# Performance work log

Hardware: AMD Instinct MI355X
Metric: run time of the kernel (lower is better)

## Reference

```python
import jax, jax.numpy as jnp
import numpy as np

THETA = 10000.0
D_K = 64
NUM_HEADS = 16


def _rope_tables(token_positions):
    # token_positions: [s] int -> cos/sin: [s, d_k//2]
    pos = token_positions.astype(jnp.float32)
    dim_idx = jnp.arange(0, D_K, 2, dtype=jnp.float32)
    freqs = 1.0 / (THETA ** (dim_idx / D_K))  # [d_k//2]
    ang = pos[:, None] * freqs[None, :]       # [s, d_k//2]
    return jnp.cos(ang), jnp.sin(ang)


def _apply_rope(x, cos, sin):
    # x: [b, h, s, d_k]; cos/sin: [s, d_k//2] broadcast over b, h
    x1 = x[..., 0::2]
    x2 = x[..., 1::2]
    r1 = x1 * cos - x2 * sin
    r2 = x2 * cos + x1 * sin
    return jnp.stack([r1, r2], axis=-1).reshape(x.shape)


def setup_inputs() -> dict:
    key = jax.random.key(0)
    ks = jax.random.split(key, 5)
    b, s, d = 2, 2048, 1024
    x = jax.random.normal(ks[0], (b, s, d), dtype=jnp.float32)
    token_positions = jnp.arange(s, dtype=jnp.int32)
    scale = (2.0 / (d + d)) ** 0.5
    Wq = jax.random.normal(ks[1], (d, d), dtype=jnp.float32) * scale
    Wk = jax.random.normal(ks[2], (d, d), dtype=jnp.float32) * scale
    Wv = jax.random.normal(ks[3], (d, d), dtype=jnp.float32) * scale
    Wo = jax.random.normal(ks[4], (d, d), dtype=jnp.float32) * scale
    return {"x": x, "token_positions": token_positions,
            "Wq": Wq, "Wk": Wk, "Wv": Wv, "Wo": Wo}


def reference(x, token_positions, Wq, Wk, Wv, Wo):
    b, s, d_model = x.shape
    h, d_k = NUM_HEADS, D_K

    def split_heads(t):
        return t.reshape(b, s, h, d_k).transpose(0, 2, 1, 3)  # [b, h, s, d_k]

    Q = split_heads(jnp.einsum('ij,bsj->bsi', Wq, x))
    K = split_heads(jnp.einsum('ij,bsj->bsi', Wk, x))
    V = split_heads(jnp.einsum('ij,bsj->bsi', Wv, x))

    cos, sin = _rope_tables(token_positions)
    Q = _apply_rope(Q, cos, sin)
    K = _apply_rope(K, cos, sin)

    scale = 1.0 / jnp.sqrt(jnp.float32(d_k))
    scores = jnp.einsum('bhqd,bhkd->bhqk', Q, K) * scale  # [b, h, s, s]
    causal = jnp.tril(jnp.ones((s, s), dtype=bool))
    scores = jnp.where(causal, scores, -jnp.inf)
    attn = jax.nn.softmax(scores, axis=-1)
    out = jnp.einsum('bhqk,bhkd->bhqd', attn, V)
    out = out.transpose(0, 2, 1, 3).reshape(b, s, d_model)
    return jnp.einsum('ij,bsj->bsi', Wo, out)
```

## Files before the change

### kernel.cpp

```cpp
#include <hip/hip_runtime.h>
#include <hip/hip_bf16.h>


typedef __attribute__((ext_vector_type(8))) __bf16 bf16x8;
typedef __attribute__((ext_vector_type(4))) float f32x4;
typedef __attribute__((ext_vector_type(16))) float f32x16;
typedef __attribute__((ext_vector_type(4))) int int4v;
typedef __attribute__((ext_vector_type(2))) unsigned int uint2v;

#define MFMA16(a, b, c) __builtin_amdgcn_mfma_f32_16x16x32_bf16(a, b, c, 0, 0, 0)
#define MFMA32(a, b, c) __builtin_amdgcn_mfma_f32_32x32x16_bf16(a, b, c, 0, 0, 0)

__device__ inline unsigned short f2b(float f) {
  unsigned u = __builtin_bit_cast(unsigned, f);
  u = (u + 0x7FFF + ((u >> 16) & 1)) >> 16;
  return (unsigned short)u;
}

__device__ inline unsigned pk2b(float lo, float hi) {
  return (unsigned)f2b(lo) | ((unsigned)f2b(hi) << 16);
}

__device__ inline unsigned cvtpk(float lo, float hi) {
  unsigned r;
  asm("v_cvt_pk_bf16_f32 %0, %1, %2" : "=v"(r) : "v"(lo), "v"(hi));
  return r;
}

__device__ inline void plswap(unsigned a, unsigned b, unsigned& o0, unsigned& o1) {
#if __has_builtin(__builtin_amdgcn_permlane32_swap)
  auto r = __builtin_amdgcn_permlane32_swap(a, b, false, false);
  o0 = r[0];
  o1 = r[1];
#else
  unsigned sa = (unsigned)__shfl_xor((int)a, 32, 64);
  unsigned sb = (unsigned)__shfl_xor((int)b, 32, 64);
  bool hi = (threadIdx.x & 32) != 0;
  o0 = hi ? sb : a;
  o1 = hi ? b : sa;
#endif
}

__device__ inline float fexp2(float x) {
#if __has_builtin(__builtin_amdgcn_exp2f)
  return __builtin_amdgcn_exp2f(x);
#else
  return exp2f(x);
#endif
}


__device__ inline void cvt4(const float* __restrict__ s, unsigned short* __restrict__ d,
                            int i, float sc) {
  float4 v = *(const float4*)(s + i);
  uint2v p = {pk2b(v.x * sc, v.y * sc), pk2b(v.z * sc, v.w * sc)};
  *(uint2v*)(d + i) = p;
}

__global__ __launch_bounds__(256) void prep_kernel(
    const float* __restrict__ x, const float* __restrict__ Wq,
    const float* __restrict__ Wk, const float* __restrict__ Wv,
    const float* __restrict__ Wo, const int* __restrict__ tp,
    unsigned short* __restrict__ xb, unsigned short* __restrict__ Wqkvb,
    unsigned short* __restrict__ Wob, float* __restrict__ cosT,
    float* __restrict__ sinT) {
  int t = blockIdx.x * 256 + threadIdx.x;
  if (t < 1048576) {
    cvt4(x, xb, t * 4, 1.0f);
  } else if (t < 1310720) {
    cvt4(Wq, Wqkvb, (t - 1048576) * 4, 0.18033688f);
  } else if (t < 1572864) {
    cvt4(Wk, Wqkvb + 1048576, (t - 1310720) * 4, 1.0f);
  } else if (t < 1835008) {
    cvt4(Wv, Wqkvb + 2097152, (t - 1572864) * 4, 1.0f);
  } else if (t < 2097152) {
    cvt4(Wo, Wob, (t - 1835008) * 4, 1.0f);
  } else {
    int base = (t - 2097152) * 4;
#pragma unroll
    for (int j = 0; j < 4; ++j) {
      int idx = base + j;
      int p = idx >> 5, i = idx & 31;
      float pos = (float)tp[p];
      float freq = powf(10000.0f, -(float)i / 32.0f);
      float ang = pos * freq;
      cosT[idx] = cosf(ang);
      sinT[idx] = sinf(ang);
    }
  }
}


__device__ __forceinline__ void g_stage(const unsigned short* __restrict__ A,
                                        const unsigned short* __restrict__ B,
                                        unsigned short* __restrict__ As,
                                        unsigned short* __restrict__ Bs,
                                        int m0, int n0, int k0, int w, int lane) {
  const int srow = lane >> 3;
  const int schunk = (lane & 7) ^ srow;
#pragma unroll
  for (int c = 0; c < 4; ++c) {
    const int rb = w * 32 + c * 8;
    const unsigned short* ga = A + (size_t)(m0 + rb + srow) * 1024 + k0 + schunk * 8;
    __builtin_amdgcn_global_load_lds(
        (const __attribute__((address_space(1))) void*)ga,
        (__attribute__((address_space(3))) void*)(As + rb * 64), 16, 0, 0);
    const int rl = rb + srow;
    const int rB = n0 + (rl & 96) + ((rl & 15) << 1) + ((rl >> 4) & 1);
    const unsigned short* gb = B + (size_t)rB * 1024 + k0 + schunk * 8;
    __builtin_amdgcn_global_load_lds(
        (const __attribute__((address_space(1))) void*)gb,
        (__attribute__((address_space(3))) void*)(Bs + rb * 64), 16, 0, 0);
  }
}


__global__ __launch_bounds__(256) void gemm_qkv_kernel(
    const unsigned short* __restrict__ A,
    const unsigned short* __restrict__ B,
    unsigned short* __restrict__ Qb, unsigned short* __restrict__ Kb,
    unsigned short* __restrict__ VbT,
    const float* __restrict__ cosT, const float* __restrict__ sinT) {
  __shared__ unsigned short As[2][128 * 64];
  __shared__ unsigned short Bs[2][128 * 64];
  const int bid = blockIdx.x;
  const int sw = (bid & 7) * 96 + (bid >> 3);
  const int n0 = (sw % 24) * 128, m0 = (sw / 24) * 128;
  const int tid = threadIdx.x, w = tid >> 6, lane = tid & 63;
  const int l15 = lane & 15, l4 = lane >> 4;
  const int wr = w >> 1, wc = w & 1;

  f32x4 acc[4][4] = {};

  g_stage(A, B, As[0], Bs[0], m0, n0, 0, w, lane);
  asm volatile("s_waitcnt vmcnt(0)" ::: "memory");
  __builtin_amdgcn_s_barrier();

  int cur = 0;
  for (int k0 = 0; k0 < 1024; k0 += 64) {
    if (k0 + 64 < 1024)
      g_stage(A, B, As[cur ^ 1], Bs[cur ^ 1], m0, n0, k0 + 64, w, lane);
#pragma unroll
    for (int kk = 0; kk < 2; ++kk) {
      bf16x8 af[4], bfr[4];
#pragma unroll
      for (int m = 0; m < 4; m++) {
        const int row = wr * 64 + m * 16 + l15;
        af[m] = *(const bf16x8*)(&As[cur][row * 64 + (((kk * 4 + l4) ^ (l15 & 7)) * 8)]);
      }
#pragma unroll
      for (int n = 0; n < 4; n++) {
        const int row = wc * 64 + n * 16 + l15;
        bfr[n] = *(const bf16x8*)(&Bs[cur][row * 64 + (((kk * 4 + l4) ^ (l15 & 7)) * 8)]);
      }
#pragma unroll
      for (int m = 0; m < 4; m++)
#pragma unroll
        for (int n = 0; n < 4; n++)
          acc[m][n] = MFMA16(af[m], bfr[n], acc[m][n]);
    }
    asm volatile("s_waitcnt vmcnt(0)" ::: "memory");
    __builtin_amdgcn_s_barrier();
    cur ^= 1;
  }

  const int cbase = n0 & 1023;
  if (n0 < 2048) {
    unsigned short* dst = (n0 < 1024) ? Qb : Kb;
#pragma unroll
    for (int m = 0; m < 4; m++) {
      const int row0 = m0 + wr * 64 + m * 16 + l4 * 4;
#pragma unroll
      for (int k = 0; k < 2; k++) {
        const int col = cbase + wc * 64 + k * 32 + 2 * l15;
        const int pi = k * 16 + l15;
#pragma unroll
        for (int r = 0; r < 4; r++) {
          const int pos = (row0 + r) & 2047;
          float c = cosT[pos * 32 + pi], s = sinT[pos * 32 + pi];
          float v0 = acc[m][2 * k][r], v1 = acc[m][2 * k + 1][r];
          float r1 = fmaf(v0, c, -v1 * s);
          float r2 = fmaf(v1, c, v0 * s);
          *(unsigned*)(dst + (size_t)(row0 + r) * 1024 + col) = pk2b(r1, r2);
        }
      }
    }
  } else {
#pragma unroll
    for (int m = 0; m < 4; m++) {
      const int row0 = m0 + wr * 64 + m * 16 + l4 * 4;
      const int bb = row0 >> 11, seq = row0 & 2047;
#pragma unroll
      for (int k = 0; k < 2; k++) {
        const int dkg = cbase + wc * 64 + k * 32 + 2 * l15;
        const int h = dkg >> 6, dk = dkg & 63;
        unsigned short* vp = VbT + (size_t)(bb * 16 + h) * 131072 + dk * 2048 + seq;
        uint2v e = {pk2b(acc[m][2 * k][0], acc[m][2 * k][1]),
                    pk2b(acc[m][2 * k][2], acc[m][2 * k][3])};
        *(uint2v*)vp = e;
        uint2v o = {pk2b(acc[m][2 * k + 1][0], acc[m][2 * k + 1][1]),
                    pk2b(acc[m][2 * k + 1][2], acc[m][2 * k + 1][3])};
        *(uint2v*)(vp + 2048) = o;
      }
    }
  }
}


__global__ __launch_bounds__(256) void gemm_out_kernel(
    const unsigned short* __restrict__ A,
    const unsigned short* __restrict__ B,
    float* __restrict__ out) {
  __shared__ unsigned short As[2][128 * 64];
  __shared__ unsigned short Bs[2][128 * 64];
  const int bid = blockIdx.x;
  const int sw = (bid & 7) * 32 + (bid >> 3);
  const int n0 = (sw % 8) * 128, m0 = (sw / 8) * 128;
  const int tid = threadIdx.x, w = tid >> 6, lane = tid & 63;
  const int l15 = lane & 15, l4 = lane >> 4;
  const int wr = w >> 1, wc = w & 1;

  f32x4 acc[4][4] = {};

  g_stage(A, B, As[0], Bs[0], m0, n0, 0, w, lane);
  asm volatile("s_waitcnt vmcnt(0)" ::: "memory");
  __builtin_amdgcn_s_barrier();

  int cur = 0;
  for (int k0 = 0; k0 < 1024; k0 += 64) {
    if (k0 + 64 < 1024)
      g_stage(A, B, As[cur ^ 1], Bs[cur ^ 1], m0, n0, k0 + 64, w, lane);
#pragma unroll
    for (int kk = 0; kk < 2; ++kk) {
      bf16x8 af[4], bfr[4];
#pragma unroll
      for (int m = 0; m < 4; m++) {
        const int row = wr * 64 + m * 16 + l15;
        af[m] = *(const bf16x8*)(&As[cur][row * 64 + (((kk * 4 + l4) ^ (l15 & 7)) * 8)]);
      }
#pragma unroll
      for (int n = 0; n < 4; n++) {
        const int row = wc * 64 + n * 16 + l15;
        bfr[n] = *(const bf16x8*)(&Bs[cur][row * 64 + (((kk * 4 + l4) ^ (l15 & 7)) * 8)]);
      }
#pragma unroll
      for (int m = 0; m < 4; m++)
#pragma unroll
        for (int n = 0; n < 4; n++)
          acc[m][n] = MFMA16(af[m], bfr[n], acc[m][n]);
    }
    asm volatile("s_waitcnt vmcnt(0)" ::: "memory");
    __builtin_amdgcn_s_barrier();
    cur ^= 1;
  }

#pragma unroll
  for (int m = 0; m < 4; m++) {
    const int row0 = m0 + wr * 64 + m * 16 + l4 * 4;
#pragma unroll
    for (int k = 0; k < 2; k++) {
      const int col = n0 + wc * 64 + k * 32 + 2 * l15;
#pragma unroll
      for (int r = 0; r < 4; r++) {
        float2 v = {acc[m][2 * k][r], acc[m][2 * k + 1][r]};
        *(float2*)(out + (size_t)(row0 + r) * 1024 + col) = v;
      }
    }
  }
}


__device__ __forceinline__ void stage_tiles(const unsigned short* __restrict__ Kgb,
                                            const unsigned short* __restrict__ Vgb,
                                            unsigned short* KsBuf, unsigned short* VsBuf,
                                            int kv0, int w, int lane) {
#pragma unroll
  for (int c = 0; c < 2; ++c) {
    const int rowbase = w * 16 + c * 8;
    const int row = rowbase + (lane >> 3);
    const int chunk = (lane & 7) ^ (lane >> 3);
    const unsigned short* gk = Kgb + (size_t)(kv0 + row) * 1024 + chunk * 8;
    __builtin_amdgcn_global_load_lds(
        (const __attribute__((address_space(1))) void*)gk,
        (__attribute__((address_space(3))) void*)(KsBuf + rowbase * 64), 16, 0, 0);
    const unsigned short* gv = Vgb + (size_t)row * 2048 + kv0 + chunk * 8;
    __builtin_amdgcn_global_load_lds(
        (const __attribute__((address_space(1))) void*)gv,
        (__attribute__((address_space(3))) void*)(VsBuf + rowbase * 64), 16, 0, 0);
  }
}

__global__ __launch_bounds__(256) void attn_kernel(
    const unsigned short* __restrict__ Qb,
    const unsigned short* __restrict__ Kb,
    const unsigned short* __restrict__ VbT,
    unsigned short* __restrict__ Ob) {
  __shared__ unsigned short Ks[3][64 * 64];
  __shared__ unsigned short Vs[3][64 * 64];
  const int bh = blockIdx.x;
  const int y = blockIdx.y;
  const int qt = (y < 8) ? (15 - 2 * y) : (2 * (y - 8));
  const int b = bh >> 4, h = bh & 15;
  const int tid = threadIdx.x, w = tid >> 6, lane = tid & 63;
  const int l31 = lane & 31, l32 = lane >> 5;
  const int sw = l31 & 7;

  const unsigned short* qptr =
      Qb + (size_t)(b * 2048 + qt * 128 + w * 32 + l31) * 1024 + h * 64 + l32 * 8;
  bf16x8 qa[4];
#pragma unroll
  for (int kk = 0; kk < 4; ++kk) qa[kk] = *(const bf16x8*)(qptr + kk * 16);

  f32x16 oacc[2] = {};
  float m = -3e38f, l = 0.f;

  const unsigned short* Kgb = Kb + (size_t)b * 2048 * 1024 + h * 64;
  const unsigned short* Vgb = VbT + (size_t)bh * 131072;

  const int nt = 2 * qt + 2;
  stage_tiles(Kgb, Vgb, Ks[0], Vs[0], 0, w, lane);
  stage_tiles(Kgb, Vgb, Ks[1], Vs[1], 64, w, lane);

  int ib = 0, is_ = 2;
  for (int t = 0; t < nt; ++t) {
    if (t < nt - 1) {
      asm volatile("s_waitcnt vmcnt(4)" ::: "memory");
    } else {
      asm volatile("s_waitcnt vmcnt(0)" ::: "memory");
    }
    __builtin_amdgcn_s_barrier();
    __builtin_amdgcn_sched_barrier(0);
    if (t + 2 < nt)
      stage_tiles(Kgb, Vgb, Ks[is_], Vs[is_], (t + 2) * 64, w, lane);

    const char* ksb = (const char*)Ks[ib];
    f32x16 st[2];
    __builtin_amdgcn_s_setprio(1);
#pragma unroll
    for (int f = 0; f < 2; ++f) {
      const char* kb = ksb + (f * 32 + l31) * 128;
      f32x16 z = {};
#pragma unroll
      for (int kk = 0; kk < 4; ++kk) {
        bf16x8 kf = *(const bf16x8*)(kb + ((((kk << 1) | l32) ^ sw) * 16));
        z = MFMA32(kf, qa[kk], z);
      }
      st[f] = z;
    }
    __builtin_amdgcn_s_setprio(0);

    if (t >= 2 * qt + (w >> 1)) {
      const int qg = qt * 128 + w * 32 + l31;
      const int kvb = t * 64 + 4 * l32;
#pragma unroll
      for (int f = 0; f < 2; ++f)
#pragma unroll
        for (int reg = 0; reg < 16; ++reg) {
          int kv = kvb + 32 * f + (reg & 3) + 8 * (reg >> 2);
          if (kv > qg) st[f][reg] = -3e38f;
        }
    }

    float a8[8];
#pragma unroll
    for (int j = 0; j < 8; ++j)
      a8[j] = fmaxf(fmaxf(st[0][j], st[0][j + 8]), fmaxf(st[1][j], st[1][j + 8]));
    float pm = fmaxf(fmaxf(fmaxf(a8[0], a8[1]), fmaxf(a8[2], a8[3])),
                     fmaxf(fmaxf(a8[4], a8[5]), fmaxf(a8[6], a8[7])));
    pm = fmaxf(pm, __shfl_xor(pm, 32, 64));

    if (!__all(pm - m <= 8.0f)) {
      float mn = fmaxf(m, pm);
      float al = fexp2(m - mn);
      l *= al;
#pragma unroll
      for (int df = 0; df < 2; ++df)
#pragma unroll
        for (int reg = 0; reg < 16; ++reg) oacc[df][reg] *= al;
      m = mn;
    }

    unsigned pku[2][4][2];
    float rs0 = 0.f, rs1 = 0.f;
#pragma unroll
    for (int f = 0; f < 2; ++f)
#pragma unroll
      for (int rr = 0; rr < 4; ++rr)
#pragma unroll
        for (int i = 0; i < 2; ++i) {
          float p0 = fexp2(st[f][4 * rr + 2 * i] - m);
          float p1 = fexp2(st[f][4 * rr + 2 * i + 1] - m);
          rs0 += p0; rs1 += p1;
          pku[f][rr][i] = cvtpk(p0, p1);
        }
    float rs = rs0 + rs1;
    rs += __shfl_xor(rs, 32, 64);
    l += rs;

    union FB { unsigned u[4]; bf16x8 v; };
    FB pfrag[4];
#pragma unroll
    for (int kk = 0; kk < 4; ++kk) {
      const int f = kk >> 1, kl = kk & 1;
      unsigned o00, o10, o01, o11;
      plswap(pku[f][2 * kl][0], pku[f][2 * kl + 1][0], o00, o10);
      plswap(pku[f][2 * kl][1], pku[f][2 * kl + 1][1], o01, o11);
      pfrag[kk].u[0] = o00; pfrag[kk].u[1] = o01;
      pfrag[kk].u[2] = o10; pfrag[kk].u[3] = o11;
    }

    const char* vsb = (const char*)Vs[ib];
    __builtin_amdgcn_s_setprio(1);
#pragma unroll
    for (int df = 0; df < 2; ++df) {
      const char* vb = vsb + (df * 32 + l31) * 128;
#pragma unroll
      for (int kk = 0; kk < 4; ++kk) {
        bf16x8 vf = *(const bf16x8*)(vb + ((((kk << 1) | l32) ^ sw) * 16));
        oacc[df] = MFMA32(vf, pfrag[kk].v, oacc[df]);
      }
    }
    __builtin_amdgcn_s_setprio(0);

    ib = (ib == 2) ? 0 : ib + 1;
    is_ = (is_ == 2) ? 0 : is_ + 1;
  }

  const float inv = 1.0f / l;
  unsigned short* ob =
      Ob + (size_t)(b * 2048 + qt * 128 + w * 32 + l31) * 1024 + h * 64 + 4 * l32;
#pragma unroll
  for (int df = 0; df < 2; ++df)
#pragma unroll
    for (int rr = 0; rr < 4; ++rr)
#pragma unroll
      for (int i = 0; i < 2; ++i) {
        *(unsigned*)(ob + df * 32 + rr * 8 + 2 * i) =
            pk2b(oacc[df][4 * rr + 2 * i] * inv, oacc[df][4 * rr + 2 * i + 1] * inv);
      }
}


extern "C" void kernel_launch(void* const* d_in, const int* in_sizes, int n_in,
                              void* d_out, int out_size, void* d_ws, size_t ws_size,
                              hipStream_t stream) {
  (void)in_sizes; (void)n_in; (void)out_size; (void)ws_size;
  const float* x  = (const float*)d_in[0];
  const int*  tp  = (const int*)d_in[1];
  const float* Wq = (const float*)d_in[2];
  const float* Wk = (const float*)d_in[3];
  const float* Wv = (const float*)d_in[4];
  const float* Wo = (const float*)d_in[5];
  float* out = (float*)d_out;

  char* ws = (char*)d_ws;
  unsigned short* xb    = (unsigned short*)(ws);
  unsigned short* Ob    = (unsigned short*)(ws);
  unsigned short* Wqkvb = (unsigned short*)(ws + (8ull << 20));
  unsigned short* Wob   = (unsigned short*)(ws + (14ull << 20));
  unsigned short* Qb    = (unsigned short*)(ws + (16ull << 20));
  unsigned short* Kb    = (unsigned short*)(ws + (24ull << 20));
  unsigned short* VbT   = (unsigned short*)(ws + (32ull << 20));
  float* cosT = (float*)(ws + (40ull << 20));
  float* sinT = (float*)(ws + (40ull << 20) + 2048 * 32 * 4);

  prep_kernel<<<8256, 256, 0, stream>>>(x, Wq, Wk, Wv, Wo, tp, xb, Wqkvb, Wob, cosT, sinT);
  gemm_qkv_kernel<<<768, 256, 0, stream>>>(xb, Wqkvb, Qb, Kb, VbT, cosT, sinT);
  attn_kernel<<<dim3(32, 16), 256, 0, stream>>>(Qb, Kb, VbT, Ob);
  gemm_out_kernel<<<256, 256, 0, stream>>>(Ob, Wob, out);
}
```

Baseline: 125.4 us.

## Split long causal query tiles across two blocks and merge partial softmax results

Reworks the causal attention work split so that each block pair handles one long query tile split at a KV boundary plus one short tile. The first half processes the long tile's first part and then a short tile, and the second half processes the remainder of the long tile. Partial outputs and (m, l) stats are written to workspace and combined by a new merge kernel. The aim is balanced per-block work and less tail imbalance, at the cost of an extra kernel launch, bf16 round-trips of partial outputs, and a launch_bounds occupancy hint of 2.

```diff
diff --git a/kernel.cpp b/kernel.cpp
--- a/kernel.cpp
+++ b/kernel.cpp
@@ -15,6 +15,10 @@
   unsigned u = __builtin_bit_cast(unsigned, f);
   u = (u + 0x7FFF + ((u >> 16) & 1)) >> 16;
   return (unsigned short)u;
+}
+
+__device__ inline float b2f(unsigned short u) {
+  return __builtin_bit_cast(float, ((unsigned)u) << 16);
 }
 
 __device__ inline unsigned pk2b(float lo, float hi) {
@@ -290,18 +294,15 @@
   }
 }
 
-__global__ __launch_bounds__(256) void attn_kernel(
+__device__ __forceinline__ void attn_stream(
+    int qt, int t0, int t1, bool finalize,
+    int b, int h, int w, int lane,
     const unsigned short* __restrict__ Qb,
-    const unsigned short* __restrict__ Kb,
-    const unsigned short* __restrict__ VbT,
-    unsigned short* __restrict__ Ob) {
-  __shared__ unsigned short Ks[3][64 * 64];
-  __shared__ unsigned short Vs[3][64 * 64];
-  const int bh = blockIdx.x;
-  const int y = blockIdx.y;
-  const int qt = (y < 8) ? (15 - 2 * y) : (2 * (y - 8));
-  const int b = bh >> 4, h = bh & 15;
-  const int tid = threadIdx.x, w = tid >> 6, lane = tid & 63;
+    const unsigned short* __restrict__ Kgb,
+    const unsigned short* __restrict__ Vgb,
+    unsigned short* __restrict__ outBase, int ostride,
+    float* __restrict__ statsOut,
+    unsigned short (*Ks)[64 * 64], unsigned short (*Vs)[64 * 64]) {
   const int l31 = lane & 31, l32 = lane >> 5;
   const int sw = l31 & 7;
 
@@ -314,23 +315,19 @@
   f32x16 oacc[2] = {};
   float m = -3e38f, l = 0.f;
 
-  const unsigned short* Kgb = Kb + (size_t)b * 2048 * 1024 + h * 64;
-  const unsigned short* Vgb = VbT + (size_t)bh * 131072;
-
-  const int nt = 2 * qt + 2;
-  stage_tiles(Kgb, Vgb, Ks[0], Vs[0], 0, w, lane);
-  stage_tiles(Kgb, Vgb, Ks[1], Vs[1], 64, w, lane);
+  stage_tiles(Kgb, Vgb, Ks[0], Vs[0], t0 * 64, w, lane);
+  stage_tiles(Kgb, Vgb, Ks[1], Vs[1], (t0 + 1) * 64, w, lane);
 
   int ib = 0, is_ = 2;
-  for (int t = 0; t < nt; ++t) {
-    if (t < nt - 1) {
+  for (int t = t0; t < t1; ++t) {
+    if (t < t1 - 1) {
       asm volatile("s_waitcnt vmcnt(4)" ::: "memory");
     } else {
       asm volatile("s_waitcnt vmcnt(0)" ::: "memory");
     }
     __builtin_amdgcn_s_barrier();
     __builtin_amdgcn_sched_barrier(0);
-    if (t + 2 < nt)
+    if (t + 2 < t1)
       stage_tiles(Kgb, Vgb, Ks[is_], Vs[is_], (t + 2) * 64, w, lane);
 
     const char* ksb = (const char*)Ks[ib];
@@ -426,9 +423,8 @@
     is_ = (is_ == 2) ? 0 : is_ + 1;
   }
 
-  const float inv = 1.0f / l;
-  unsigned short* ob =
-      Ob + (size_t)(b * 2048 + qt * 128 + w * 32 + l31) * 1024 + h * 64 + 4 * l32;
+  const float sc = finalize ? (1.0f / l) : 1.0f;
+  unsigned short* ob = outBase + (size_t)(w * 32 + l31) * ostride + 4 * l32;
 #pragma unroll
   for (int df = 0; df < 2; ++df)
 #pragma unroll
@@ -436,8 +432,83 @@
 #pragma unroll
       for (int i = 0; i < 2; ++i) {
         *(unsigned*)(ob + df * 32 + rr * 8 + 2 * i) =
-            pk2b(oacc[df][4 * rr + 2 * i] * inv, oacc[df][4 * rr + 2 * i + 1] * inv);
-      }
+            pk2b(oacc[df][4 * rr + 2 * i] * sc, oacc[df][4 * rr + 2 * i + 1] * sc);
+      }
+  if (!finalize && l32 == 0) {
+    float2 st2 = {m, l};
+    *(float2*)(statsOut + (w * 32 + l31) * 2) = st2;
+  }
+}
+
+__global__ __launch_bounds__(256, 2) void attn_kernel(
+    const unsigned short* __restrict__ Qb,
+    const unsigned short* __restrict__ Kb,
+    const unsigned short* __restrict__ VbT,
+    unsigned short* __restrict__ Ob,
+    unsigned short* __restrict__ P2,
+    float* __restrict__ stats1, float* __restrict__ stats2) {
+  __shared__ unsigned short Ks[3][64 * 64];
+  __shared__ unsigned short Vs[3][64 * 64];
+  const int bh = blockIdx.x;
+  const int y = blockIdx.y;
+  const int j = y >> 1, half = y & 1;
+  const int b = bh >> 4, h = bh & 15;
+  const int qtB = 15 - j;
+  const int x = 15 - 2 * j;
+  const int cid = bh * 8 + j;
+  const int tid = threadIdx.x, w = tid >> 6, lane = tid & 63;
+
+  const unsigned short* Kgb = Kb + (size_t)b * 2048 * 1024 + h * 64;
+  const unsigned short* Vgb = VbT + (size_t)bh * 131072;
+
+  if (half == 0) {
+    attn_stream(qtB, 0, x, false, b, h, w, lane, Qb, Kgb, Vgb,
+                Ob + (size_t)(b * 2048 + qtB * 128) * 1024 + h * 64, 1024,
+                stats1 + cid * 256, Ks, Vs);
+    __syncthreads();
+    attn_stream(j, 0, 2 * j + 2, true, b, h, w, lane, Qb, Kgb, Vgb,
+                Ob + (size_t)(b * 2048 + j * 128) * 1024 + h * 64, 1024,
+                nullptr, Ks, Vs);
+  } else {
+    attn_stream(qtB, x, 32 - 2 * j, false, b, h, w, lane, Qb, Kgb, Vgb,
+                P2 + (size_t)cid * 8192, 64,
+                stats2 + cid * 256, Ks, Vs);
+  }
+}
+
+
+__global__ __launch_bounds__(256) void merge_kernel(
+    unsigned short* __restrict__ Ob, const unsigned short* __restrict__ P2,
+    const float* __restrict__ stats1, const float* __restrict__ stats2) {
+  const int cid = blockIdx.x;
+  const int bh = cid >> 3, j = cid & 7, qt = 15 - j;
+  const int b = bh >> 4, h = bh & 15;
+  const int tid = threadIdx.x;
+  const int r = tid >> 1, ch = (tid & 1) * 32;
+
+  const float m1 = stats1[cid * 256 + r * 2], l1 = stats1[cid * 256 + r * 2 + 1];
+  const float m2 = stats2[cid * 256 + r * 2], l2 = stats2[cid * 256 + r * 2 + 1];
+  const float M = fmaxf(m1, m2);
+  const float a1 = fexp2(m1 - M), a2 = fexp2(m2 - M);
+  const float invL = 1.0f / (l1 * a1 + l2 * a2);
+  const float c1 = a1 * invL, c2 = a2 * invL;
+
+  unsigned short* o1 = Ob + (size_t)(b * 2048 + qt * 128 + r) * 1024 + h * 64 + ch;
+  const unsigned short* o2 = P2 + (size_t)cid * 8192 + r * 64 + ch;
+#pragma unroll
+  for (int i = 0; i < 32; i += 8) {
+    int4v v1 = *(const int4v*)(o1 + i);
+    int4v v2 = *(const int4v*)(o2 + i);
+    int4v ro;
+#pragma unroll
+    for (int k = 0; k < 4; ++k) {
+      unsigned u1 = (unsigned)v1[k], u2 = (unsigned)v2[k];
+      float lo = b2f((unsigned short)u1) * c1 + b2f((unsigned short)u2) * c2;
+      float hi = b2f((unsigned short)(u1 >> 16)) * c1 + b2f((unsigned short)(u2 >> 16)) * c2;
+      ro[k] = (int)pk2b(lo, hi);
+    }
+    *(int4v*)(o1 + i) = ro;
+  }
 }
 
 
@@ -457,15 +528,19 @@
   unsigned short* xb    = (unsigned short*)(ws);
   unsigned short* Ob    = (unsigned short*)(ws);
   unsigned short* Wqkvb = (unsigned short*)(ws + (8ull << 20));
+  unsigned short* P2    = (unsigned short*)(ws + (8ull << 20));
   unsigned short* Wob   = (unsigned short*)(ws + (14ull << 20));
   unsigned short* Qb    = (unsigned short*)(ws + (16ull << 20));
   unsigned short* Kb    = (unsigned short*)(ws + (24ull << 20));
   unsigned short* VbT   = (unsigned short*)(ws + (32ull << 20));
-  float* cosT = (float*)(ws + (40ull << 20));
-  float* sinT = (float*)(ws + (40ull << 20) + 2048 * 32 * 4);
+  float* cosT   = (float*)(ws + (40ull << 20));
+  float* sinT   = (float*)(ws + (40ull << 20) + 262144);
+  float* stats1 = (float*)(ws + (40ull << 20));
+  float* stats2 = (float*)(ws + (40ull << 20) + 262144);
 
   prep_kernel<<<8256, 256, 0, stream>>>(x, Wq, Wk, Wv, Wo, tp, xb, Wqkvb, Wob, cosT, sinT);
   gemm_qkv_kernel<<<768, 256, 0, stream>>>(xb, Wqkvb, Qb, Kb, VbT, cosT, sinT);
-  attn_kernel<<<dim3(32, 16), 256, 0, stream>>>(Qb, Kb, VbT, Ob);
+  attn_kernel<<<dim3(32, 16), 256, 0, stream>>>(Qb, Kb, VbT, Ob, P2, stats1, stats2);
+  merge_kernel<<<256, 256, 0, stream>>>(Ob, P2, stats1, stats2);
   gemm_out_kernel<<<256, 256, 0, stream>>>(Ob, Wob, out);
 }
```

Result: faster. 113.9 us (-9.1%).
